# Kernel optimization log

Measured on AMD Instinct MI355X. Metric: run time of the kernel, lower is better.

The kernel has to match this reference:

```python
import jax, jax.numpy as jnp
import numpy as np

B, H, W, C = 8, 64, 64, 256
CK = C // 8  # key/query dim of conv_f / conv_g


def setup_inputs() -> dict:
    key = jax.random.key(0)
    ks = jax.random.split(key, 10)
    s = lambda fan_in: 1.0 / np.sqrt(fan_in)
    return {
        "x": jax.random.normal(ks[0], (B, H, W, C), dtype=jnp.float32),
        "Wf": jax.random.normal(ks[1], (C, CK), dtype=jnp.float32) * s(C),
        "bf": jnp.zeros((CK,), dtype=jnp.float32),
        "Wg": jax.random.normal(ks[2], (C, CK), dtype=jnp.float32) * s(C),
        "bg": jnp.zeros((CK,), dtype=jnp.float32),
        "Wh": jax.random.normal(ks[3], (C, C), dtype=jnp.float32) * s(C),
        "bh": jnp.zeros((C,), dtype=jnp.float32),
        "Wo": jax.random.normal(ks[4], (C, C), dtype=jnp.float32) * s(C),
        "bo": jnp.zeros((C,), dtype=jnp.float32),
        # original init is zeros; use a random scalar so output/grads are nontrivial
        "gamma": jax.random.normal(ks[5], (1,), dtype=jnp.float32),
    }


def reference(x, Wf, bf, Wg, bg, Wh, bh, Wo, bo, gamma):
    b, h, w, c = x.shape
    n = h * w
    xf = x.reshape(b, n, c)                       # flatten spatial: [B, N, C]
    # 1x1 convs == per-pixel matmuls
    f = xf @ Wf + bf                              # [B, N, C//8]
    g = xf @ Wg + bg                              # [B, N, C//8]
    hh = xf @ Wh + bh                             # [B, N, C]
    # scores[b, i, j] = <g_i, f_j>; softmax over j (keys)
    scores = jnp.einsum("bnd,bmd->bnm", g, f)     # [B, N, N]
    attn = jax.nn.softmax(scores, axis=-1)
    o = jnp.einsum("bnm,bmc->bnc", attn, hh)      # [B, N, C]
    o = o @ Wo + bo                               # conv_o (1x1)
    out = gamma * o + xf                          # gamma residual
    return out.reshape(b, h, w, c)
```

## Files before the change

kernel.cpp:

```cpp
#include <hip/hip_runtime.h>
#include <hip/hip_fp16.h>
#include <hip/hip_bf16.h>

constexpr int BB  = 8;
constexpr int NN  = 4096;
constexpr int CC  = 256;
constexpr int CKK = 32;

typedef __attribute__((ext_vector_type(8))) short    short8;
typedef __attribute__((ext_vector_type(8))) _Float16 half8;
typedef __attribute__((ext_vector_type(4))) _Float16 half4;
typedef __attribute__((ext_vector_type(4))) float    f32x4;

__device__ __forceinline__ unsigned short bf16_bits(float v) {
    __hip_bfloat16 h = __float2bfloat16(v);
    return *reinterpret_cast<unsigned short*>(&h);
}
__device__ __forceinline__ float bf16_val(unsigned short u) {
    __hip_bfloat16 h = *reinterpret_cast<__hip_bfloat16*>(&u);
    return __bfloat162float(h);
}

__global__ __launch_bounds__(256) void prep_kernel(
    const float* __restrict__ Wf, const float* __restrict__ Wg,
    const float* __restrict__ Wh, const float* __restrict__ Wo,
    unsigned short* __restrict__ WThi, unsigned short* __restrict__ WTlo)
{
    const int n = blockIdx.x;
    const int k = threadIdx.x;
    float v;
    if      (n < 256) v = Wh[k * 256 + n];
    else if (n < 288) v = Wf[k * 32 + (n - 256)];
    else if (n < 320) v = Wg[k * 32 + (n - 288)];
    else              v = Wo[k * 256 + (n - 320)];
    const unsigned short hi = bf16_bits(v);
    WThi[n * 256 + k] = hi;
    WTlo[n * 256 + k] = bf16_bits(v - bf16_val(hi));
}

__global__ __launch_bounds__(256) void fgh_kernel(
    const float* __restrict__ x,
    const unsigned short* __restrict__ WThi, const unsigned short* __restrict__ WTlo,
    const float* __restrict__ bf, const float* __restrict__ bg,
    const float* __restrict__ bh,
    _Float16* __restrict__ fbuf, _Float16* __restrict__ gbuf,
    _Float16* __restrict__ hhT)
{
    __shared__ __align__(16) float XT[2][64 * 36];

    const int tid = threadIdx.x, w = tid >> 6, lane = tid & 63;
    const int ln = lane & 15, lq = lane >> 4;
    const int b  = blockIdx.x & 7;
    const int q0 = (blockIdx.x >> 3) * 64;
    const size_t px0 = (size_t)b * NN + q0;
    const int n0 = w * 80;

    const int p  = tid >> 2;
    const int jq = tid & 3;
    const float* xrow = &x[(px0 + p) * CC + jq * 8];

    f32x4 acc[4][5];
    #pragma unroll
    for (int i = 0; i < 4; ++i)
        #pragma unroll
        for (int j = 0; j < 5; ++j) acc[i][j] = {0.f, 0.f, 0.f, 0.f};

    short8 Ahi[4], Alo[4];
    float4 ra0 = *(const float4*)&xrow[0];
    float4 ra1 = *(const float4*)&xrow[4];

    int cur = 0;
    #pragma unroll 1
    for (int kc = 0; kc < 8; ++kc) {
        const int k0 = kc * 32;
        float* dst = &XT[cur][p * 36 + jq * 8];
        *(float4*)&dst[0] = ra0;
        *(float4*)&dst[4] = ra1;
        __syncthreads();
        if (kc < 7) {
            ra0 = *(const float4*)&xrow[(kc + 1) * 32];
            ra1 = *(const float4*)&xrow[(kc + 1) * 32 + 4];
        }
        #pragma unroll
        for (int mt = 0; mt < 4; ++mt) {
            float av[8];
            const float* sp = &XT[cur][(mt * 16 + ln) * 36 + lq * 8];
            *(float4*)&av[0] = *(const float4*)&sp[0];
            *(float4*)&av[4] = *(const float4*)&sp[4];
            #pragma unroll
            for (int j = 0; j < 8; ++j) {
                const unsigned short h = bf16_bits(av[j]);
                Ahi[mt][j] = (short)h;
                Alo[mt][j] = (short)bf16_bits(av[j] - bf16_val(h));
            }
        }
        #pragma unroll
        for (int nt = 0; nt < 5; ++nt) {
            const size_t boff = (size_t)(n0 + nt * 16 + ln) * 256 + k0 + lq * 8;
            const short8 Bhi = *(const short8*)&WThi[boff];
            const short8 Blo = *(const short8*)&WTlo[boff];
            #pragma unroll
            for (int mt = 0; mt < 4; ++mt) {
                acc[mt][nt] = __builtin_amdgcn_mfma_f32_16x16x32_bf16(Ahi[mt], Bhi, acc[mt][nt], 0, 0, 0);
                acc[mt][nt] = __builtin_amdgcn_mfma_f32_16x16x32_bf16(Ahi[mt], Blo, acc[mt][nt], 0, 0, 0);
                acc[mt][nt] = __builtin_amdgcn_mfma_f32_16x16x32_bf16(Alo[mt], Bhi, acc[mt][nt], 0, 0, 0);
            }
        }
        cur ^= 1;
    }

    _Float16* st = (_Float16*)&XT[0][0] + w * 1088;
    const int rr = lane >> 3, k8 = lane & 7;

    #pragma unroll
    for (int nt = 0; nt < 5; ++nt) {
        const int cbase = n0 + nt * 16;
        const int c = cbase + ln;
        if (cbase < 256) {
            const float bias = bh[c];
            #pragma unroll
            for (int mt = 0; mt < 4; ++mt) {
                half4 hv;
                #pragma unroll
                for (int r = 0; r < 4; ++r) hv[r] = (_Float16)(acc[mt][nt][r] + bias);
                *(half4*)&st[ln * 68 + mt * 16 + lq * 4] = hv;
            }
            #pragma unroll
            for (int i = 0; i < 2; ++i) {
                const half8 row = *(const half8*)&st[(i * 8 + rr) * 68 + k8 * 8];
                *(half8*)&hhT[((size_t)(b * CC + cbase + i * 8 + rr)) * NN + q0 + k8 * 8] = row;
            }
        } else {
            const bool isf = (c < 288);
            const int d = isf ? (c - 256) : (c - 288);
            const float bias = isf ? bf[d] : bg[d];
            _Float16* dst2 = isf ? fbuf : gbuf;
            #pragma unroll
            for (int mt = 0; mt < 4; ++mt)
                #pragma unroll
                for (int r = 0; r < 4; ++r)
                    dst2[(px0 + mt * 16 + lq * 4 + r) * CKK + d] =
                        (_Float16)(acc[mt][nt][r] + bias);
        }
    }
}

__global__ __launch_bounds__(256, 2) void attn_kernel(
    const _Float16* __restrict__ fbuf, const _Float16* __restrict__ gbuf,
    const _Float16* __restrict__ hhT,
    const unsigned short* __restrict__ WThi, const unsigned short* __restrict__ WTlo,
    const float* __restrict__ bo, const float* __restrict__ gamma,
    const float* __restrict__ x, float* __restrict__ out)
{
    __shared__ __align__(16) float OF[64 * 268];
    _Float16* P0 = (_Float16*)OF;
    _Float16* P1 = P0 + 64 * 72;
    __shared__ float mxbuf[4][64];
    __shared__ float rsbuf[4][64];

    const int tid = threadIdx.x, w = tid >> 6, lane = tid & 63;
    const int ln = lane & 15, lq = lane >> 4;
    const int b  = blockIdx.x & 7;
    const int q0 = (blockIdx.x >> 3) * 64;
    const int cb = w * 64;

    const f32x4 zero = {0.f, 0.f, 0.f, 0.f};
    constexpr float LOG2E = 1.4426950408889634f;

    half8 Bg[4];
    #pragma unroll
    for (int qt = 0; qt < 4; ++qt)
        Bg[qt] = *(const half8*)&gbuf[(size_t)(b * NN + q0 + qt * 16 + ln) * CKK + lq * 8];

    const _Float16* fb = &fbuf[(size_t)(b * NN + w * 16 + ln) * CKK + lq * 8];
    const _Float16* hb = &hhT[((size_t)(b * CC + cb + ln)) * NN + lq * 8];

    float mx[4];
    #pragma unroll
    for (int qt = 0; qt < 4; ++qt) mx[qt] = -1e30f;
    half8 Afc = *(const half8*)fb;
    #pragma unroll 1
    for (int j0 = 0; j0 < NN; j0 += 64) {
        const int jn = (j0 + 64 < NN) ? j0 + 64 : j0;
        const half8 Afn = *(const half8*)&fb[(size_t)jn * CKK];
        #pragma unroll
        for (int qt = 0; qt < 4; ++qt) {
            const f32x4 s = __builtin_amdgcn_mfma_f32_16x16x32_f16(Afc, Bg[qt], zero, 0, 0, 0);
            mx[qt] = fmaxf(mx[qt], fmaxf(fmaxf(s[0], s[1]), fmaxf(s[2], s[3])));
        }
        Afc = Afn;
    }
    #pragma unroll
    for (int qt = 0; qt < 4; ++qt) {
        mx[qt] = fmaxf(mx[qt], __shfl_xor(mx[qt], 16));
        mx[qt] = fmaxf(mx[qt], __shfl_xor(mx[qt], 32));
    }
    if (lane < 16) {
        #pragma unroll
        for (int qt = 0; qt < 4; ++qt) mxbuf[w][qt * 16 + ln] = mx[qt];
    }
    __syncthreads();
    float mk[4];
    #pragma unroll
    for (int qt = 0; qt < 4; ++qt)
        mk[qt] = LOG2E * fmaxf(fmaxf(mxbuf[0][qt * 16 + ln], mxbuf[1][qt * 16 + ln]),
                               fmaxf(mxbuf[2][qt * 16 + ln], mxbuf[3][qt * 16 + ln]));

    f32x4 O[4][4];
    #pragma unroll
    for (int qt = 0; qt < 4; ++qt)
        #pragma unroll
        for (int ct = 0; ct < 4; ++ct) O[qt][ct] = zero;
    float psum[4] = {0.f, 0.f, 0.f, 0.f};

    auto phaseA = [&](const half8& Af, _Float16* Pb) {
        #pragma unroll
        for (int qt = 0; qt < 4; ++qt) {
            const f32x4 s = __builtin_amdgcn_mfma_f32_16x16x32_f16(Af, Bg[qt], zero, 0, 0, 0);
            half4 ph;
            float ps = 0.f;
            #pragma unroll
            for (int r = 0; r < 4; ++r) {
                const float p = exp2f(fmaf(s[r], LOG2E, -mk[qt]));
                ps += p;
                ph[r] = (_Float16)p;
            }
            psum[qt] += ps;
            *(half4*)&Pb[(qt * 16 + ln) * 72 + w * 16 + lq * 4] = ph;
        }
    };

    auto loadBh = [&](half8 (&Bh)[4][2], int j0) {
        #pragma unroll
        for (int ct = 0; ct < 4; ++ct)
            #pragma unroll
            for (int kh = 0; kh < 2; ++kh)
                Bh[ct][kh] = *(const half8*)&hb[(size_t)ct * 16 * NN + j0 + kh * 32];
    };

    auto phaseB = [&](const half8 (&Bh)[4][2], const _Float16* Pb) {
        __builtin_amdgcn_s_setprio(1);
        #pragma unroll
        for (int qt = 0; qt < 4; ++qt) {
            const half8 Ap0 = *(const half8*)&Pb[(qt * 16 + ln) * 72 + lq * 8];
            const half8 Ap1 = *(const half8*)&Pb[(qt * 16 + ln) * 72 + 32 + lq * 8];
            #pragma unroll
            for (int ct = 0; ct < 4; ++ct) {
                O[qt][ct] = __builtin_amdgcn_mfma_f32_16x16x32_f16(Ap0, Bh[ct][0], O[qt][ct], 0, 0, 0);
                O[qt][ct] = __builtin_amdgcn_mfma_f32_16x16x32_f16(Ap1, Bh[ct][1], O[qt][ct], 0, 0, 0);
            }
        }
        __builtin_amdgcn_s_setprio(0);
    };

    half8 Bh0[4][2], Bh1[4][2];
    half8 Af0, Af1;
    loadBh(Bh0, 0);
    Af0 = *(const half8*)fb;

    #pragma unroll 1
    for (int j0 = 0; j0 < NN; j0 += 128) {
        phaseA(Af0, P0);
        __syncthreads();
        loadBh(Bh1, j0 + 64);
        Af1 = *(const half8*)&fb[(size_t)(j0 + 64) * CKK];
        phaseB(Bh0, P0);
        phaseA(Af1, P1);
        __syncthreads();
        if (j0 + 128 < NN) {
            loadBh(Bh0, j0 + 128);
            Af0 = *(const half8*)&fb[(size_t)(j0 + 128) * CKK];
        }
        phaseB(Bh1, P1);
    }

    #pragma unroll
    for (int qt = 0; qt < 4; ++qt) {
        psum[qt] += __shfl_xor(psum[qt], 16);
        psum[qt] += __shfl_xor(psum[qt], 32);
    }
    if (lane < 16) {
        #pragma unroll
        for (int qt = 0; qt < 4; ++qt) rsbuf[w][qt * 16 + ln] = psum[qt];
    }
    __syncthreads();

    #pragma unroll
    for (int qt = 0; qt < 4; ++qt)
        #pragma unroll
        for (int r = 0; r < 4; ++r) {
            const int q = qt * 16 + lq * 4 + r;
            const float rinv = 1.0f / (rsbuf[0][q] + rsbuf[1][q] + rsbuf[2][q] + rsbuf[3][q]);
            #pragma unroll
            for (int ct = 0; ct < 4; ++ct)
                OF[q * 268 + cb + ct * 16 + ln] = O[qt][ct][r] * rinv;
        }
    __syncthreads();

    {
        const int n0 = w * 64;
        f32x4 acc[4][4];
        #pragma unroll
        for (int i = 0; i < 4; ++i)
            #pragma unroll
            for (int j = 0; j < 4; ++j) acc[i][j] = {0.f, 0.f, 0.f, 0.f};

        short8 Ahi[4], Alo[4];
        #pragma unroll 1
        for (int kc = 0; kc < 8; ++kc) {
            const int k0 = kc * 32;
            #pragma unroll
            for (int mt = 0; mt < 4; ++mt) {
                float av[8];
                *(f32x4*)&av[0] = *(const f32x4*)&OF[(mt * 16 + ln) * 268 + k0 + lq * 8];
                *(f32x4*)&av[4] = *(const f32x4*)&OF[(mt * 16 + ln) * 268 + k0 + lq * 8 + 4];
                #pragma unroll
                for (int j = 0; j < 8; ++j) {
                    const unsigned short h = bf16_bits(av[j]);
                    Ahi[mt][j] = (short)h;
                    Alo[mt][j] = (short)bf16_bits(av[j] - bf16_val(h));
                }
            }
            #pragma unroll
            for (int nt = 0; nt < 4; ++nt) {
                const size_t boff = (size_t)(320 + n0 + nt * 16 + ln) * 256 + k0 + lq * 8;
                const short8 Bhi = *(const short8*)&WThi[boff];
                const short8 Blo = *(const short8*)&WTlo[boff];
                #pragma unroll
                for (int mt = 0; mt < 4; ++mt) {
                    acc[mt][nt] = __builtin_amdgcn_mfma_f32_16x16x32_bf16(Ahi[mt], Bhi, acc[mt][nt], 0, 0, 0);
                    acc[mt][nt] = __builtin_amdgcn_mfma_f32_16x16x32_bf16(Ahi[mt], Blo, acc[mt][nt], 0, 0, 0);
                    acc[mt][nt] = __builtin_amdgcn_mfma_f32_16x16x32_bf16(Alo[mt], Bhi, acc[mt][nt], 0, 0, 0);
                }
            }
        }

        const float gm = gamma[0];
        #pragma unroll
        for (int nt = 0; nt < 4; ++nt) {
            const int c = n0 + nt * 16 + ln;
            const float bias = bo[c];
            #pragma unroll
            for (int mt = 0; mt < 4; ++mt)
                #pragma unroll
                for (int r = 0; r < 4; ++r) {
                    const size_t idx = (size_t)(b * NN + q0 + mt * 16 + lq * 4 + r) * CC + c;
                    out[idx] = gm * (acc[mt][nt][r] + bias) + x[idx];
                }
        }
    }
}

extern "C" void kernel_launch(void* const* d_in, const int* in_sizes, int n_in,
                              void* d_out, int out_size, void* d_ws, size_t ws_size,
                              hipStream_t stream)
{
    (void)in_sizes; (void)n_in; (void)out_size; (void)ws_size;

    const float* x     = (const float*)d_in[0];
    const float* Wf    = (const float*)d_in[1];
    const float* bf    = (const float*)d_in[2];
    const float* Wg    = (const float*)d_in[3];
    const float* bg    = (const float*)d_in[4];
    const float* Wh    = (const float*)d_in[5];
    const float* bh    = (const float*)d_in[6];
    const float* Wo    = (const float*)d_in[7];
    const float* bo    = (const float*)d_in[8];
    const float* gamma = (const float*)d_in[9];
    float* out = (float*)d_out;

    _Float16* fbuf = (_Float16*)d_ws;
    _Float16* gbuf = fbuf + (size_t)BB * NN * CKK;
    _Float16* hhT  = gbuf + (size_t)BB * NN * CKK;
    unsigned short* WThi = (unsigned short*)(hhT + (size_t)BB * CC * NN);
    unsigned short* WTlo = WThi + (size_t)576 * 256;

    prep_kernel<<<576, 256, 0, stream>>>(Wf, Wg, Wh, Wo, WThi, WTlo);
    fgh_kernel<<<BB * NN / 64, 256, 0, stream>>>(x, WThi, WTlo, bf, bg, bh,
                                                 fbuf, gbuf, hhT);
    attn_kernel<<<BB * NN / 64, 256, 0, stream>>>(fbuf, gbuf, hhT, WThi, WTlo,
                                                  bo, gamma, x, out);
}
```

Baseline: 284.7 us.

## Split softmax row-max pass into separate key-split kernel; use native exp2

Moves the row-max pre-pass out of the attention kernel into a separate rowmax kernel. That kernel splits the 4096 keys into 4 chunks across a second grid dimension, so each block scans only a quarter of the keys. The attention kernel then reads four partial maxima from global memory instead of scanning all keys itself and syncing. It also swaps exp2f for the amdgcn exp2 builtin, which may lose a little accuracy. The cost is an extra kernel launch plus a small global write and read of the partial maxima.

```diff
diff --git a/kernel.cpp b/kernel.cpp
--- a/kernel.cpp
+++ b/kernel.cpp
@@ -19,6 +19,13 @@
 __device__ __forceinline__ float bf16_val(unsigned short u) {
     __hip_bfloat16 h = *reinterpret_cast<__hip_bfloat16*>(&u);
     return __bfloat162float(h);
+}
+__device__ __forceinline__ float exp2_x(float x) {
+#if __has_builtin(__builtin_amdgcn_exp2f)
+    return __builtin_amdgcn_exp2f(x);
+#else
+    return exp2f(x);
+#endif
 }
 
 __global__ __launch_bounds__(256) void prep_kernel(
@@ -145,9 +152,62 @@
     }
 }
 
+__global__ __launch_bounds__(256) void rowmax_kernel(
+    const _Float16* __restrict__ fbuf, const _Float16* __restrict__ gbuf,
+    float* __restrict__ mxpart)
+{
+    __shared__ float mxbuf[4][64];
+
+    const int tid = threadIdx.x, w = tid >> 6, lane = tid & 63;
+    const int ln = lane & 15, lq = lane >> 4;
+    const int b  = blockIdx.x & 7;
+    const int q0 = (blockIdx.x >> 3) * 64;
+    const int kp = blockIdx.y;
+
+    const f32x4 zero = {0.f, 0.f, 0.f, 0.f};
+
+    half8 Bg[4];
+    #pragma unroll
+    for (int qt = 0; qt < 4; ++qt)
+        Bg[qt] = *(const half8*)&gbuf[(size_t)(b * NN + q0 + qt * 16 + ln) * CKK + lq * 8];
+
+    const _Float16* fb = &fbuf[(size_t)(b * NN + kp * 1024 + w * 16 + ln) * CKK + lq * 8];
+
+    float mx[4];
+    #pragma unroll
+    for (int qt = 0; qt < 4; ++qt) mx[qt] = -1e30f;
+    half8 Afc = *(const half8*)fb;
+    #pragma unroll 1
+    for (int j0 = 0; j0 < 1024; j0 += 64) {
+        const int jn = (j0 + 64 < 1024) ? j0 + 64 : j0;
+        const half8 Afn = *(const half8*)&fb[(size_t)jn * CKK];
+        #pragma unroll
+        for (int qt = 0; qt < 4; ++qt) {
+            const f32x4 s = __builtin_amdgcn_mfma_f32_16x16x32_f16(Afc, Bg[qt], zero, 0, 0, 0);
+            mx[qt] = fmaxf(mx[qt], fmaxf(fmaxf(s[0], s[1]), fmaxf(s[2], s[3])));
+        }
+        Afc = Afn;
+    }
+    #pragma unroll
+    for (int qt = 0; qt < 4; ++qt) {
+        mx[qt] = fmaxf(mx[qt], __shfl_xor(mx[qt], 16));
+        mx[qt] = fmaxf(mx[qt], __shfl_xor(mx[qt], 32));
+    }
+    if (lane < 16) {
+        #pragma unroll
+        for (int qt = 0; qt < 4; ++qt) mxbuf[w][qt * 16 + ln] = mx[qt];
+    }
+    __syncthreads();
+    if (tid < 64) {
+        const float m = fmaxf(fmaxf(mxbuf[0][tid], mxbuf[1][tid]),
+                              fmaxf(mxbuf[2][tid], mxbuf[3][tid]));
+        mxpart[(size_t)kp * (BB * NN) + (size_t)b * NN + q0 + tid] = m;
+    }
+}
+
 __global__ __launch_bounds__(256, 2) void attn_kernel(
     const _Float16* __restrict__ fbuf, const _Float16* __restrict__ gbuf,
-    const _Float16* __restrict__ hhT,
+    const _Float16* __restrict__ hhT, const float* __restrict__ mxpart,
     const unsigned short* __restrict__ WThi, const unsigned short* __restrict__ WTlo,
     const float* __restrict__ bo, const float* __restrict__ gamma,
     const float* __restrict__ x, float* __restrict__ out)
@@ -155,7 +215,6 @@
     __shared__ __align__(16) float OF[64 * 268];
     _Float16* P0 = (_Float16*)OF;
     _Float16* P1 = P0 + 64 * 72;
-    __shared__ float mxbuf[4][64];
     __shared__ float rsbuf[4][64];
 
     const int tid = threadIdx.x, w = tid >> 6, lane = tid & 63;
@@ -175,36 +234,14 @@
     const _Float16* fb = &fbuf[(size_t)(b * NN + w * 16 + ln) * CKK + lq * 8];
     const _Float16* hb = &hhT[((size_t)(b * CC + cb + ln)) * NN + lq * 8];
 
-    float mx[4];
-    #pragma unroll
-    for (int qt = 0; qt < 4; ++qt) mx[qt] = -1e30f;
-    half8 Afc = *(const half8*)fb;
-    #pragma unroll 1
-    for (int j0 = 0; j0 < NN; j0 += 64) {
-        const int jn = (j0 + 64 < NN) ? j0 + 64 : j0;
-        const half8 Afn = *(const half8*)&fb[(size_t)jn * CKK];
-        #pragma unroll
-        for (int qt = 0; qt < 4; ++qt) {
-            const f32x4 s = __builtin_amdgcn_mfma_f32_16x16x32_f16(Afc, Bg[qt], zero, 0, 0, 0);
-            mx[qt] = fmaxf(mx[qt], fmaxf(fmaxf(s[0], s[1]), fmaxf(s[2], s[3])));
-        }
-        Afc = Afn;
-    }
+    float mk[4];
     #pragma unroll
     for (int qt = 0; qt < 4; ++qt) {
-        mx[qt] = fmaxf(mx[qt], __shfl_xor(mx[qt], 16));
-        mx[qt] = fmaxf(mx[qt], __shfl_xor(mx[qt], 32));
-    }
-    if (lane < 16) {
-        #pragma unroll
-        for (int qt = 0; qt < 4; ++qt) mxbuf[w][qt * 16 + ln] = mx[qt];
-    }
-    __syncthreads();
-    float mk[4];
-    #pragma unroll
-    for (int qt = 0; qt < 4; ++qt)
-        mk[qt] = LOG2E * fmaxf(fmaxf(mxbuf[0][qt * 16 + ln], mxbuf[1][qt * 16 + ln]),
-                               fmaxf(mxbuf[2][qt * 16 + ln], mxbuf[3][qt * 16 + ln]));
+        const float* mp = &mxpart[(size_t)b * NN + q0 + qt * 16 + ln];
+        const float m = fmaxf(fmaxf(mp[0], mp[BB * NN]),
+                              fmaxf(mp[2 * (BB * NN)], mp[3 * (BB * NN)]));
+        mk[qt] = LOG2E * m;
+    }
 
     f32x4 O[4][4];
     #pragma unroll
@@ -221,7 +258,7 @@
             float ps = 0.f;
             #pragma unroll
             for (int r = 0; r < 4; ++r) {
-                const float p = exp2f(fmaf(s[r], LOG2E, -mk[qt]));
+                const float p = exp2_x(fmaf(s[r], LOG2E, -mk[qt]));
                 ps += p;
                 ph[r] = (_Float16)p;
             }
@@ -374,10 +411,12 @@
     _Float16* hhT  = gbuf + (size_t)BB * NN * CKK;
     unsigned short* WThi = (unsigned short*)(hhT + (size_t)BB * CC * NN);
     unsigned short* WTlo = WThi + (size_t)576 * 256;
+    float* mxpart = (float*)(WTlo + (size_t)576 * 256);
 
     prep_kernel<<<576, 256, 0, stream>>>(Wf, Wg, Wh, Wo, WThi, WTlo);
     fgh_kernel<<<BB * NN / 64, 256, 0, stream>>>(x, WThi, WTlo, bf, bg, bh,
                                                  fbuf, gbuf, hhT);
-    attn_kernel<<<BB * NN / 64, 256, 0, stream>>>(fbuf, gbuf, hhT, WThi, WTlo,
+    rowmax_kernel<<<dim3(BB * NN / 64, 4), 256, 0, stream>>>(fbuf, gbuf, mxpart);
+    attn_kernel<<<BB * NN / 64, 256, 0, stream>>>(fbuf, gbuf, hhT, mxpart, WThi, WTlo,
                                                   bo, gamma, x, out);
 }
```

Measured after the change: 282.2 us. About the same (-0.9%).
